# Kernel tuning notes

Hardware: AMD Instinct MI355X
Metric: run time of the kernel (lower is better)

Reference implementation:

```python
import jax, jax.numpy as jnp
import numpy as np

B, N = 8, 64            # batch, max boxes per image
H, W = 152, 272         # heatmap size (input 608x1088, stride 4)
IMG_H, IMG_W = 608, 1088
EMB_DIM, NUM_CLASSES = 128, 500
K, SIGMA = 5, 3.0
EPS = 1e-4


def setup_inputs() -> dict:
    key = jax.random.key(0)
    ks = jax.random.split(key, 10)
    heatmap_head = jax.random.normal(ks[0], (B, 1, H, W), jnp.float32)
    box_sizes_head = jax.random.normal(ks[1], (B, 2, H, W), jnp.float32)
    center_offsets_head = jax.random.normal(ks[2], (B, 2, H, W), jnp.float32)
    reid_head = jax.random.normal(ks[3], (B, EMB_DIM, H, W), jnp.float32) * 0.1
    # ground truth boxes: (id, xc, yc, w, h), centers on distinct cells to avoid scatter collisions
    tid = jax.random.randint(ks[4], (B, N, 1), 1, NUM_CLASSES + 1).astype(jnp.float32)
    perm = jax.vmap(lambda k: jax.random.permutation(k, H * W)[:N])(jax.random.split(ks[5], B))
    rowi = (perm // W).astype(jnp.float32)
    coli = (perm % W).astype(jnp.float32)
    sub = jax.random.uniform(ks[6], (B, N, 2), minval=0.1, maxval=0.9)
    xc = (coli + sub[..., 0]) / W
    yc = (rowi + sub[..., 1]) / H
    wh = jax.random.uniform(ks[7], (B, N, 2), minval=0.01, maxval=0.2)
    ground_truth = jnp.concatenate(
        [tid, xc[..., None], yc[..., None], wh], axis=-1).astype(jnp.float32)
    W_cls = jax.random.normal(ks[8], (NUM_CLASSES, EMB_DIM), jnp.float32) / np.sqrt(EMB_DIM)
    b_cls = jnp.zeros((NUM_CLASSES,), jnp.float32)
    return dict(heatmap_head=heatmap_head, box_sizes_head=box_sizes_head,
                center_offsets_head=center_offsets_head, reid_head=reid_head,
                ground_truth=ground_truth, W_cls=W_cls, b_cls=b_cls)


def _gauss_kernel():
    g = jnp.exp(-(((jnp.arange(K, dtype=jnp.float32) - (K - 1) / 2) / SIGMA) ** 2) / 2)
    return jnp.outer(g, g)[None, None]  # [1,1,5,5], unnormalized, peak 1


def reference(heatmap_head, box_sizes_head, center_offsets_head, reid_head,
              ground_truth, W_cls, b_cls):
    pred_hm = jnp.clip(jax.nn.sigmoid(heatmap_head), EPS, 1.0 - EPS)

    tid = ground_truth[..., 0]
    xc, yc = ground_truth[..., 1], ground_truth[..., 2]
    bw, bh = ground_truth[..., 3], ground_truth[..., 4]

    row_f, col_f = yc * H, xc * W
    rr = jnp.clip(jnp.floor(row_f).astype(jnp.int32), 0, H - 1).ravel()
    cc = jnp.clip(jnp.floor(col_f).astype(jnp.int32), 0, W - 1).ravel()
    bb = jnp.broadcast_to(jnp.arange(B)[:, None], (B, N)).ravel()

    gt_bs = (jnp.zeros((B, 2, H, W), jnp.float32)
             .at[bb, 0, rr, cc].set((bh * IMG_H).ravel())
             .at[bb, 1, rr, cc].set((bw * IMG_W).ravel()))
    gt_off = (jnp.zeros((B, 2, H, W), jnp.float32)
              .at[bb, 0, rr, cc].set((row_f - jnp.floor(row_f)).ravel())
              .at[bb, 1, rr, cc].set((col_f - jnp.floor(col_f)).ravel()))
    mask = jnp.zeros((B, 1, H, W), jnp.float32).at[bb, 0, rr, cc].set(1.0)

    gt_hm = jax.lax.conv_general_dilated(mask, _gauss_kernel(), (1, 1), 'SAME')

    # focal loss (alpha=2, beta=4)
    pos = (gt_hm == 1.0).astype(jnp.float32)
    neg = (gt_hm < 1.0).astype(jnp.float32)
    pos_loss = ((1.0 - pred_hm) ** 2 * jnp.log(pred_hm) * pos).sum()
    neg_loss = ((1.0 - gt_hm) ** 4 * pred_hm ** 2 * jnp.log(1.0 - pred_hm) * neg).sum()
    npos = pos.sum()
    hm_loss = jnp.where(npos >= 1.0, -(pos_loss + neg_loss) / npos, -neg_loss)

    # masked L1 (sum reduction); mask broadcasts over the 2 channels
    bs_loss = (jnp.abs(box_sizes_head - gt_bs) * mask).sum()
    off_loss = (jnp.abs(center_offsets_head - gt_off) * mask).sum()

    # reid: gather features at centers, classify, mean CE per sample, summed over batch
    feats = reid_head[bb, :, rr, cc]                     # [B*N, emb]
    logits = feats @ W_cls.T + b_cls                     # [B*N, num_classes]
    labels = jnp.where(tid.ravel() > NUM_CLASSES, NUM_CLASSES - 1,
                       tid.ravel() - 1).astype(jnp.int32)
    logp = jax.nn.log_softmax(logits, axis=-1)
    ce = -jnp.take_along_axis(logp, labels[:, None], axis=1)[:, 0]
    reid_loss = ce.reshape(B, N).mean(axis=1).sum()

    det_loss = 1.0 * hm_loss + 0.1 * bs_loss + 1.0 * off_loss
    total = 1.0 * det_loss + 1.0 * reid_loss
    # sorted keys: box_sizes, center_offsets, detection, heatmap, reid, total
    return (bs_loss, off_loss, det_loss, hm_loss, reid_loss, total)
```

## Files before the change

### kernel.cpp

```cpp
#include <hip/hip_runtime.h>

#define Bb 8
#define Nn 64
#define Hh 152
#define Ww 272
#define HW (Hh * Ww)
#define EMB 128
#define NC 500
#define EPSV 1e-4f

#define HM_BLOCKS 256
#define SAMP_BLOCKS 64
#define TOTAL_BLOCKS (HM_BLOCKS + SAMP_BLOCKS)

__global__ void main_kernel(const float* __restrict__ hm,
                            const float* __restrict__ bs,
                            const float* __restrict__ off,
                            const float* __restrict__ reid,
                            const float* __restrict__ gt,
                            const float* __restrict__ Wc,
                            const float* __restrict__ bc,
                            float* __restrict__ partials) {
    __shared__ int   s_r[Nn];
    __shared__ int   s_c[Nn];
    __shared__ float s_feat[EMB];
    __shared__ float s_log[NC];
    __shared__ float s_max4[4];
    __shared__ float s_sum4[4];

    const int gb = blockIdx.x;
    const int t = threadIdx.x;
    const int wave = t >> 6;
    const int lane = t & 63;

    float out0 = 0.0f, out1 = 0.0f, out2 = 0.0f,
          out3 = 0.0f, out4 = 0.0f, out5 = 0.0f;

    if (gb < HM_BLOCKS) {
        const int b = gb >> 5;
        const int tile = gb & 31;

        if (t < Nn) {
            const float* g5 = gt + ((size_t)b * Nn + t) * 5;
            float rf = g5[2] * (float)Hh;
            float cf = g5[1] * (float)Ww;
            int rr = (int)floorf(rf); rr = min(max(rr, 0), Hh - 1);
            int cc = (int)floorf(cf); cc = min(max(cc, 0), Ww - 1);
            s_r[t] = rr;
            s_c[t] = cc;
        }
        __syncthreads();

        float g[5];
#pragma unroll
        for (int i = 0; i < 5; ++i) {
            float tv = (float)(i - 2) / 3.0f;
            g[i] = expf(-0.5f * tv * tv);
        }

        float pos_l = 0.0f, neg_l = 0.0f, np = 0.0f;
        const float* hmb = hm + (size_t)b * HW;

        for (int p = tile * 256 + t; p < HW; p += 32 * 256) {
            int y = p / Ww;
            int x = p - y * Ww;
            float h = hmb[p];
            float pred = 1.0f / (1.0f + expf(-h));
            pred = fminf(fmaxf(pred, EPSV), 1.0f - EPSV);

            float gh = 0.0f;
#pragma unroll 8
            for (int n = 0; n < Nn; ++n) {
                int dy = y - s_r[n];
                int dx = x - s_c[n];
                if (dy >= -2 && dy <= 2 && dx >= -2 && dx <= 2)
                    gh += g[dy + 2] * g[dx + 2];
            }

            if (gh == 1.0f) {
                float om = 1.0f - pred;
                pos_l += om * om * logf(pred);
                np += 1.0f;
            } else if (gh < 1.0f) {
                float om = 1.0f - gh;
                float w = om * om;
                w = w * w;
                neg_l += w * pred * pred * logf(1.0f - pred);
            }
        }

#pragma unroll
        for (int o = 32; o > 0; o >>= 1) {
            pos_l += __shfl_down(pos_l, o);
            neg_l += __shfl_down(neg_l, o);
            np    += __shfl_down(np, o);
        }
        if (lane == 0) {
            s_log[wave]      = pos_l;
            s_log[wave + 4]  = neg_l;
            s_log[wave + 8]  = np;
        }
        __syncthreads();
        if (t == 0) {
            out2 = s_log[0] + s_log[1] + s_log[2] + s_log[3];
            out3 = s_log[4] + s_log[5] + s_log[6] + s_log[7];
            out4 = s_log[8] + s_log[9] + s_log[10] + s_log[11];
        }
    } else {
        const int sblk = gb - HM_BLOCKS;
        const int b = sblk >> 3;
        const int n0 = (sblk & 7) * 8;

        float ce_sum = 0.0f, bl_sum = 0.0f, ol_sum = 0.0f;

        for (int i = 0; i < 8; ++i) {
            const int s = b * Nn + n0 + i;
            const float* g5 = gt + (size_t)s * 5;
            const float tf = g5[0];
            const float xc = g5[1], yc = g5[2];
            const float bw = g5[3], bh = g5[4];

            const float rf = yc * (float)Hh;
            const float cf = xc * (float)Ww;
            const float fr = floorf(rf);
            const float fc = floorf(cf);
            const int rr = min(max((int)fr, 0), Hh - 1);
            const int cc = min(max((int)fc, 0), Ww - 1);
            const size_t pix = (size_t)rr * Ww + cc;

            __syncthreads();
            if (t < EMB)
                s_feat[t] = reid[(size_t)b * EMB * HW + (size_t)t * HW + pix];
            __syncthreads();

            float lmax = -INFINITY;
            const float4* f4 = (const float4*)s_feat;
#pragma unroll
            for (int half = 0; half < 2; ++half) {
                const int c = t + half * 256;
                if (c < NC) {
                    const float4* wr = (const float4*)(Wc + (size_t)c * EMB);
                    float d = bc[c];
#pragma unroll 8
                    for (int k = 0; k < EMB / 4; ++k) {
                        float4 w4 = wr[k];
                        float4 fv = f4[k];
                        d += w4.x * fv.x + w4.y * fv.y
                           + w4.z * fv.z + w4.w * fv.w;
                    }
                    s_log[c] = d;
                    lmax = fmaxf(lmax, d);
                }
            }

#pragma unroll
            for (int o = 32; o > 0; o >>= 1)
                lmax = fmaxf(lmax, __shfl_xor(lmax, o));
            if (lane == 0) s_max4[wave] = lmax;
            __syncthreads();
            const float mv = fmaxf(fmaxf(s_max4[0], s_max4[1]),
                                   fmaxf(s_max4[2], s_max4[3]));

            float lsum = 0.0f;
#pragma unroll
            for (int half = 0; half < 2; ++half) {
                const int c = t + half * 256;
                if (c < NC) lsum += expf(s_log[c] - mv);
            }
#pragma unroll
            for (int o = 32; o > 0; o >>= 1)
                lsum += __shfl_xor(lsum, o);
            if (lane == 0) s_sum4[wave] = lsum;
            __syncthreads();

            if (t == 0) {
                const float tot = s_sum4[0] + s_sum4[1] + s_sum4[2] + s_sum4[3];
                int lab = (tf > (float)NC) ? (NC - 1) : ((int)tf - 1);
                lab = min(max(lab, 0), NC - 1);
                ce_sum += logf(tot) + mv - s_log[lab];

                const float* bsb = bs  + (size_t)b * 2 * HW;
                const float* ofb = off + (size_t)b * 2 * HW;
                bl_sum += fabsf(bsb[pix]      - bh * 608.0f)
                        + fabsf(bsb[HW + pix] - bw * 1088.0f);
                ol_sum += fabsf(ofb[pix]      - (rf - fr))
                        + fabsf(ofb[HW + pix] - (cf - fc));
            }
        }
        if (t == 0) {
            out0 = bl_sum;
            out1 = ol_sum;
            out5 = ce_sum;
        }
    }

    if (t == 0) {
        float* row = partials + (size_t)gb * 8;
        row[0] = out0; row[1] = out1; row[2] = out2; row[3] = out3;
        row[4] = out4; row[5] = out5; row[6] = 0.0f; row[7] = 0.0f;
    }
}

__global__ void final_kernel(const float* __restrict__ partials,
                             float* __restrict__ out) {
    __shared__ float s_fin[4][6];
    const int t = threadIdx.x;
    const int wave = t >> 6;
    const int lane = t & 63;

    float v[6] = {0, 0, 0, 0, 0, 0};
    for (int r = t; r < TOTAL_BLOCKS; r += 256) {
        const float* row = partials + (size_t)r * 8;
#pragma unroll
        for (int j = 0; j < 6; ++j) v[j] += row[j];
    }
#pragma unroll
    for (int o = 32; o > 0; o >>= 1)
#pragma unroll
        for (int j = 0; j < 6; ++j) v[j] += __shfl_xor(v[j], o);
    if (lane == 0)
#pragma unroll
        for (int j = 0; j < 6; ++j) s_fin[wave][j] = v[j];
    __syncthreads();

    if (t == 0) {
        float a[6];
#pragma unroll
        for (int j = 0; j < 6; ++j)
            a[j] = s_fin[0][j] + s_fin[1][j] + s_fin[2][j] + s_fin[3][j];
        const float bsl = a[0], ofl = a[1], pl = a[2],
                    nl = a[3], np = a[4], re = a[5];
        const float hmv   = (np >= 1.0f) ? (-(pl + nl) / np) : (-nl);
        const float reidl = re / (float)Nn;
        const float det   = hmv + 0.1f * bsl + ofl;
        out[0] = bsl;
        out[1] = ofl;
        out[2] = det;
        out[3] = hmv;
        out[4] = reidl;
        out[5] = det + reidl;
    }
}

extern "C" void kernel_launch(void* const* d_in, const int* in_sizes, int n_in,
                              void* d_out, int out_size, void* d_ws, size_t ws_size,
                              hipStream_t stream) {
    const float* hm   = (const float*)d_in[0];
    const float* bs   = (const float*)d_in[1];
    const float* off  = (const float*)d_in[2];
    const float* reid = (const float*)d_in[3];
    const float* gt   = (const float*)d_in[4];
    const float* Wc   = (const float*)d_in[5];
    const float* bc   = (const float*)d_in[6];
    float* out = (float*)d_out;
    float* partials = (float*)d_ws;

    hipLaunchKernelGGL(main_kernel, dim3(TOTAL_BLOCKS), dim3(256), 0, stream,
                       hm, bs, off, reid, gt, Wc, bc, partials);
    hipLaunchKernelGGL(final_kernel, dim3(1), dim3(256), 0, stream,
                       partials, out);
}
```

Baseline: 284.4 us.

## Cull boxes per row tile and split reid classification into one block per sample

Heatmap blocks now each own a contiguous band of 5 rows and use a wave ballot to build a list of only the boxes whose centers fall near that band, so each pixel loops over a few candidates instead of all 64. Sample blocks are expanded from 64 blocks of 8 sequential samples to 512 blocks of one sample each, exposing more parallelism for the gather, GEMV and softmax. The cost is more blocks and partial rows for the final reduction, plus a culling step whose correctness depends on the row-band bounds.

```diff
diff --git a/kernel.cpp b/kernel.cpp
--- a/kernel.cpp
+++ b/kernel.cpp
@@ -9,8 +9,10 @@
 #define NC 500
 #define EPSV 1e-4f
 
-#define HM_BLOCKS 256
-#define SAMP_BLOCKS 64
+#define ROWS_PER_TILE 5
+#define TILES 32
+#define HM_BLOCKS (Bb * TILES)
+#define SAMP_BLOCKS (Bb * Nn)
 #define TOTAL_BLOCKS (HM_BLOCKS + SAMP_BLOCKS)
 
 __global__ void main_kernel(const float* __restrict__ hm,
@@ -23,6 +25,9 @@
                             float* __restrict__ partials) {
     __shared__ int   s_r[Nn];
     __shared__ int   s_c[Nn];
+    __shared__ int   s_list[Nn];
+    __shared__ int   s_cnt;
+    __shared__ float s_red[12];
     __shared__ float s_feat[EMB];
     __shared__ float s_log[NC];
     __shared__ float s_max4[4];
@@ -39,6 +44,7 @@
     if (gb < HM_BLOCKS) {
         const int b = gb >> 5;
         const int tile = gb & 31;
+        const int r0 = tile * ROWS_PER_TILE;
 
         if (t < Nn) {
             const float* g5 = gt + ((size_t)b * Nn + t) * 5;
@@ -48,6 +54,13 @@
             int cc = (int)floorf(cf); cc = min(max(cc, 0), Ww - 1);
             s_r[t] = rr;
             s_c[t] = cc;
+            const bool inr = (rr >= r0 - 2) && (rr <= r0 + ROWS_PER_TILE + 1);
+            const unsigned long long m = __ballot(inr);
+            if (inr) {
+                const int idx = __popcll(m & ((1ull << t) - 1ull));
+                s_list[idx] = t;
+            }
+            if (t == 0) s_cnt = (int)__popcll(m);
         }
         __syncthreads();
 
@@ -59,33 +72,39 @@
         }
 
         float pos_l = 0.0f, neg_l = 0.0f, np = 0.0f;
-        const float* hmb = hm + (size_t)b * HW;
-
-        for (int p = tile * 256 + t; p < HW; p += 32 * 256) {
-            int y = p / Ww;
-            int x = p - y * Ww;
-            float h = hmb[p];
-            float pred = 1.0f / (1.0f + expf(-h));
-            pred = fminf(fmaxf(pred, EPSV), 1.0f - EPSV);
-
-            float gh = 0.0f;
-#pragma unroll 8
-            for (int n = 0; n < Nn; ++n) {
-                int dy = y - s_r[n];
-                int dx = x - s_c[n];
-                if (dy >= -2 && dy <= 2 && dx >= -2 && dx <= 2)
-                    gh += g[dy + 2] * g[dx + 2];
-            }
-
-            if (gh == 1.0f) {
-                float om = 1.0f - pred;
-                pos_l += om * om * logf(pred);
-                np += 1.0f;
-            } else if (gh < 1.0f) {
-                float om = 1.0f - gh;
-                float w = om * om;
-                w = w * w;
-                neg_l += w * pred * pred * logf(1.0f - pred);
+        const int rows = min(ROWS_PER_TILE, Hh - r0);
+        if (rows > 0) {
+            const float* hmb = hm + (size_t)b * HW + (size_t)r0 * Ww;
+            const int npix = rows * Ww;
+            const int cnt = s_cnt;
+
+            for (int p = t; p < npix; p += 256) {
+                int y = p / Ww;
+                int x = p - y * Ww;
+                int yy = r0 + y;
+                float h = hmb[p];
+                float pred = 1.0f / (1.0f + expf(-h));
+                pred = fminf(fmaxf(pred, EPSV), 1.0f - EPSV);
+
+                float gh = 0.0f;
+                for (int j = 0; j < cnt; ++j) {
+                    const int n = s_list[j];
+                    int dy = yy - s_r[n];
+                    int dx = x - s_c[n];
+                    if (dy >= -2 && dy <= 2 && dx >= -2 && dx <= 2)
+                        gh += g[dy + 2] * g[dx + 2];
+                }
+
+                if (gh == 1.0f) {
+                    float om = 1.0f - pred;
+                    pos_l += om * om * logf(pred);
+                    np += 1.0f;
+                } else if (gh < 1.0f) {
+                    float om = 1.0f - gh;
+                    float w = om * om;
+                    w = w * w;
+                    neg_l += w * pred * pred * logf(1.0f - pred);
+                }
             }
         }
 
@@ -96,101 +115,90 @@
             np    += __shfl_down(np, o);
         }
         if (lane == 0) {
-            s_log[wave]      = pos_l;
-            s_log[wave + 4]  = neg_l;
-            s_log[wave + 8]  = np;
+            s_red[wave]      = pos_l;
+            s_red[wave + 4]  = neg_l;
+            s_red[wave + 8]  = np;
         }
         __syncthreads();
         if (t == 0) {
-            out2 = s_log[0] + s_log[1] + s_log[2] + s_log[3];
-            out3 = s_log[4] + s_log[5] + s_log[6] + s_log[7];
-            out4 = s_log[8] + s_log[9] + s_log[10] + s_log[11];
+            out2 = s_red[0] + s_red[1] + s_red[2] + s_red[3];
+            out3 = s_red[4] + s_red[5] + s_red[6] + s_red[7];
+            out4 = s_red[8] + s_red[9] + s_red[10] + s_red[11];
         }
     } else {
-        const int sblk = gb - HM_BLOCKS;
-        const int b = sblk >> 3;
-        const int n0 = (sblk & 7) * 8;
-
-        float ce_sum = 0.0f, bl_sum = 0.0f, ol_sum = 0.0f;
-
-        for (int i = 0; i < 8; ++i) {
-            const int s = b * Nn + n0 + i;
-            const float* g5 = gt + (size_t)s * 5;
-            const float tf = g5[0];
-            const float xc = g5[1], yc = g5[2];
-            const float bw = g5[3], bh = g5[4];
-
-            const float rf = yc * (float)Hh;
-            const float cf = xc * (float)Ww;
-            const float fr = floorf(rf);
-            const float fc = floorf(cf);
-            const int rr = min(max((int)fr, 0), Hh - 1);
-            const int cc = min(max((int)fc, 0), Ww - 1);
-            const size_t pix = (size_t)rr * Ww + cc;
-
-            __syncthreads();
-            if (t < EMB)
-                s_feat[t] = reid[(size_t)b * EMB * HW + (size_t)t * HW + pix];
-            __syncthreads();
-
-            float lmax = -INFINITY;
-            const float4* f4 = (const float4*)s_feat;
-#pragma unroll
-            for (int half = 0; half < 2; ++half) {
-                const int c = t + half * 256;
-                if (c < NC) {
-                    const float4* wr = (const float4*)(Wc + (size_t)c * EMB);
-                    float d = bc[c];
+        const int s = gb - HM_BLOCKS;
+        const int b = s >> 6;
+        const int n = s & 63;
+
+        const float* g5 = gt + ((size_t)b * Nn + n) * 5;
+        const float tf = g5[0];
+        const float xc = g5[1], yc = g5[2];
+        const float bw = g5[3], bh = g5[4];
+
+        const float rf = yc * (float)Hh;
+        const float cf = xc * (float)Ww;
+        const float fr = floorf(rf);
+        const float fc = floorf(cf);
+        const int rr = min(max((int)fr, 0), Hh - 1);
+        const int cc = min(max((int)fc, 0), Ww - 1);
+        const size_t pix = (size_t)rr * Ww + cc;
+
+        if (t < EMB)
+            s_feat[t] = reid[(size_t)b * EMB * HW + (size_t)t * HW + pix];
+        __syncthreads();
+
+        float lmax = -INFINITY;
+        const float4* f4 = (const float4*)s_feat;
+#pragma unroll
+        for (int half = 0; half < 2; ++half) {
+            const int c = t + half * 256;
+            if (c < NC) {
+                const float4* wr = (const float4*)(Wc + (size_t)c * EMB);
+                float d = bc[c];
 #pragma unroll 8
-                    for (int k = 0; k < EMB / 4; ++k) {
-                        float4 w4 = wr[k];
-                        float4 fv = f4[k];
-                        d += w4.x * fv.x + w4.y * fv.y
-                           + w4.z * fv.z + w4.w * fv.w;
-                    }
-                    s_log[c] = d;
-                    lmax = fmaxf(lmax, d);
+                for (int k = 0; k < EMB / 4; ++k) {
+                    float4 w4 = wr[k];
+                    float4 fv = f4[k];
+                    d += w4.x * fv.x + w4.y * fv.y
+                       + w4.z * fv.z + w4.w * fv.w;
                 }
+                s_log[c] = d;
+                lmax = fmaxf(lmax, d);
             }
-
-#pragma unroll
-            for (int o = 32; o > 0; o >>= 1)
-                lmax = fmaxf(lmax, __shfl_xor(lmax, o));
-            if (lane == 0) s_max4[wave] = lmax;
-            __syncthreads();
-            const float mv = fmaxf(fmaxf(s_max4[0], s_max4[1]),
-                                   fmaxf(s_max4[2], s_max4[3]));
-
-            float lsum = 0.0f;
-#pragma unroll
-            for (int half = 0; half < 2; ++half) {
-                const int c = t + half * 256;
-                if (c < NC) lsum += expf(s_log[c] - mv);
-            }
-#pragma unroll
-            for (int o = 32; o > 0; o >>= 1)
-                lsum += __shfl_xor(lsum, o);
-            if (lane == 0) s_sum4[wave] = lsum;
-            __syncthreads();
-
-            if (t == 0) {
-                const float tot = s_sum4[0] + s_sum4[1] + s_sum4[2] + s_sum4[3];
-                int lab = (tf > (float)NC) ? (NC - 1) : ((int)tf - 1);
-                lab = min(max(lab, 0), NC - 1);
-                ce_sum += logf(tot) + mv - s_log[lab];
-
-                const float* bsb = bs  + (size_t)b * 2 * HW;
-                const float* ofb = off + (size_t)b * 2 * HW;
-                bl_sum += fabsf(bsb[pix]      - bh * 608.0f)
-                        + fabsf(bsb[HW + pix] - bw * 1088.0f);
-                ol_sum += fabsf(ofb[pix]      - (rf - fr))
-                        + fabsf(ofb[HW + pix] - (cf - fc));
-            }
-        }
+        }
+
+#pragma unroll
+        for (int o = 32; o > 0; o >>= 1)
+            lmax = fmaxf(lmax, __shfl_xor(lmax, o));
+        if (lane == 0) s_max4[wave] = lmax;
+        __syncthreads();
+        const float mv = fmaxf(fmaxf(s_max4[0], s_max4[1]),
+                               fmaxf(s_max4[2], s_max4[3]));
+
+        float lsum = 0.0f;
+#pragma unroll
+        for (int half = 0; half < 2; ++half) {
+            const int c = t + half * 256;
+            if (c < NC) lsum += expf(s_log[c] - mv);
+        }
+#pragma unroll
+        for (int o = 32; o > 0; o >>= 1)
+            lsum += __shfl_xor(lsum, o);
+        if (lane == 0) s_sum4[wave] = lsum;
+        __syncthreads();
+
         if (t == 0) {
-            out0 = bl_sum;
-            out1 = ol_sum;
-            out5 = ce_sum;
+            const float tot = s_sum4[0] + s_sum4[1] + s_sum4[2] + s_sum4[3];
+            int lab = (tf > (float)NC) ? (NC - 1) : ((int)tf - 1);
+            lab = min(max(lab, 0), NC - 1);
+            out5 = logf(tot) + mv - s_log[lab];
+
+            const float* bsb = bs  + (size_t)b * 2 * HW;
+            const float* ofb = off + (size_t)b * 2 * HW;
+            out0 = fabsf(bsb[pix]      - bh * 608.0f)
+                 + fabsf(bsb[HW + pix] - bw * 1088.0f);
+            out1 = fabsf(ofb[pix]      - (rf - fr))
+                 + fabsf(ofb[HW + pix] - (cf - fc));
         }
     }
 
```

Measured after the change: 230.1 us. -19.1%, faster.
